# Optimization experiments

Hardware: AMD Instinct MI355X
Metric: run time of the kernel (lower is better)

## Reference

```python
import jax, jax.numpy as jnp
import numpy as np

B, L, C, D, H = 32, 4096, 64, 512, 720
EPS = 1e-5

def _xavier(key, shape):
    fan_in, fan_out = shape
    lim = float(np.sqrt(6.0 / (fan_in + fan_out)))
    return jax.random.uniform(key, shape, minval=-lim, maxval=lim, dtype=jnp.float32)

def setup_inputs() -> dict:
    key = jax.random.key(0)
    ks = jax.random.split(key, 8)
    return {
        "x": jax.random.normal(ks[0], (B, L, C), dtype=jnp.float32),
        "alpha": jnp.full((C,), 0.5, dtype=jnp.float32),
        "rev_w": jnp.ones((C,), dtype=jnp.float32),
        "rev_b": jnp.zeros((C,), dtype=jnp.float32),
        "se_w": _xavier(ks[1], (C, D)), "se_b": jnp.zeros((D,), jnp.float32),
        "sp_w": _xavier(ks[2], (D, C)), "sp_b": jnp.zeros((C,), jnp.float32),
        "st_w": _xavier(ks[3], (L, H)), "st_b": jnp.zeros((H,), jnp.float32),
        "te_w": _xavier(ks[4], (C, D)), "te_b": jnp.zeros((D,), jnp.float32),
        "tp_w": _xavier(ks[5], (D, C)), "tp_b": jnp.zeros((C,), jnp.float32),
        "tt_w": _xavier(ks[6], (L, H)), "tt_b": jnp.zeros((H,), jnp.float32),
    }

def _path(z, ew, eb, pw, pb, tw, tb):
    # z: (B,L,C) -> embed C->D -> (identity backbone) -> proj D->C -> temporal L->H
    h = z @ ew + eb            # (B,L,D)
    h = h @ pw + pb            # (B,L,C)
    h = jnp.einsum('blc,lh->bhc', h, tw) + tb[None, :, None]  # (B,H,C)
    return h

def reference(x, alpha, rev_w, rev_b, se_w, se_b, sp_w, sp_b, st_w, st_b,
              te_w, te_b, tp_w, tp_b, tt_w, tt_b):
    # RevIN norm (stats detached, var unbiased=False)
    mean = jax.lax.stop_gradient(jnp.mean(x, axis=1, keepdims=True))          # (B,1,C)
    stdev = jax.lax.stop_gradient(jnp.sqrt(jnp.var(x, axis=1, keepdims=True) + EPS))
    xn = (x - mean) / stdev * rev_w + rev_b
    # EMA decomposition: trend[t] = a*trend[t-1] + (1-a)*x[t], trend[0]=x[0]
    a = jax.nn.sigmoid(alpha)  # (C,)
    def step(carry, xt):
        nxt = a * carry + (1.0 - a) * xt
        return nxt, nxt
    t0 = xn[:, 0]                                    # (B,C)
    _, tr = jax.lax.scan(step, t0, jnp.swapaxes(xn, 0, 1)[1:])  # (L-1,B,C)
    trend = jnp.swapaxes(jnp.concatenate([t0[None], tr], axis=0), 0, 1)  # (B,L,C)
    seasonal = xn - trend
    out = _path(seasonal, se_w, se_b, sp_w, sp_b, st_w, st_b) \
        + _path(trend,    te_w, te_b, tp_w, tp_b, tt_w, tt_b)   # (B,H,C)
    # RevIN denorm
    out = (out - rev_b) / (rev_w + EPS)
    out = out * stdev + mean
    return out
```

## Files before the change

### kernel.cpp

```cpp
#include <hip/hip_runtime.h>
#include <hip/hip_bf16.h>
#include <string.h>
#include <stdint.h>

typedef __hip_bfloat16 bf16_t;
typedef float f32x4 __attribute__((ext_vector_type(4)));
typedef short bf16x8 __attribute__((ext_vector_type(8)));

#define AS_GLOBAL __attribute__((address_space(1)))
#define AS_LDS    __attribute__((address_space(3)))

static constexpr int Bn = 32, Ln = 4096, Cn = 64, Hn = 720, HPn = 768;
static constexpr float EPSf = 1e-5f;

static constexpr size_t OSR_SLICE = (size_t)Bn * Hn * Cn;

__device__ __forceinline__ short f2bf(float f) {
  bf16_t h = __float2bfloat16(f);
  unsigned short u; memcpy(&u, &h, 2);
  return (short)u;
}

__device__ __forceinline__ float sigm(float v) { return 1.f / (1.f + expf(-v)); }

__global__ void __launch_bounds__(256) k_prep(const float* __restrict__ se_w, const float* __restrict__ sp_w,
                                              const float* __restrict__ se_b, const float* __restrict__ sp_b,
                                              const float* __restrict__ te_w, const float* __restrict__ tp_w,
                                              const float* __restrict__ te_b, const float* __restrict__ tp_b,
                                              float* __restrict__ M, float* __restrict__ cvec) {
  int p = blockIdx.y, dc = blockIdx.x, t = threadIdx.x;
  const float* ew = p ? te_w : se_w;
  const float* pw = p ? tp_w : sp_w;
  const float* eb = p ? te_b : se_b;
  const float* pb = p ? tp_b : sp_b;
  int d0 = dc * 64;
  __shared__ float ews[64][68];
  __shared__ float pws[64][68];
  __shared__ float ebs[64];
#pragma unroll
  for (int q = 0; q < 4; ++q) {
    int fi = t * 4 + q;
    int r = fi >> 4, dd = (fi * 4) & 63;
    *reinterpret_cast<f32x4*>(&ews[r][dd]) = *reinterpret_cast<const f32x4*>(&ew[r * 512 + d0 + dd]);
    int pdd = fi >> 4, c = (fi * 4) & 63;
    *reinterpret_cast<f32x4*>(&pws[pdd][c]) = *reinterpret_cast<const f32x4*>(&pw[(d0 + pdd) * 64 + c]);
  }
  if (t < 64) ebs[t] = eb[d0 + t];
  __syncthreads();
  int r0 = (t >> 4) * 4, c0 = (t & 15) * 4;
  float acc[4][4];
#pragma unroll
  for (int i = 0; i < 4; ++i)
#pragma unroll
    for (int j = 0; j < 4; ++j) acc[i][j] = 0.f;
#pragma unroll 4
  for (int g = 0; g < 16; ++g) {
    int dd = g * 4;
    f32x4 av[4], bv[4];
#pragma unroll
    for (int i = 0; i < 4; ++i) av[i] = *reinterpret_cast<const f32x4*>(&ews[r0 + i][dd]);
#pragma unroll
    for (int d = 0; d < 4; ++d) bv[d] = *reinterpret_cast<const f32x4*>(&pws[dd + d][c0]);
#pragma unroll
    for (int d = 0; d < 4; ++d)
#pragma unroll
      for (int i = 0; i < 4; ++i)
#pragma unroll
        for (int j = 0; j < 4; ++j) acc[i][j] = fmaf(av[i][d], bv[d][j], acc[i][j]);
  }
#pragma unroll
  for (int i = 0; i < 4; ++i)
#pragma unroll
    for (int j = 0; j < 4; ++j)
      atomicAdd(&M[p * 4096 + (r0 + i) * 64 + c0 + j], acc[i][j]);
  if (t < 64) {
    float s = (dc == 0) ? pb[t] : 0.f;
#pragma unroll 8
    for (int dd = 0; dd < 64; ++dd) s = fmaf(ebs[dd], pws[dd][t], s);
    atomicAdd(&cvec[p * 64 + t], s);
  }
}

__global__ void k_wprep(const float* __restrict__ st_w, const float* __restrict__ tt_w,
                        bf16_t* __restrict__ Wt, float* __restrict__ S) {
  int p = blockIdx.z;
  const float* W = p ? tt_w : st_w;
  int l0 = blockIdx.x * 64, h0 = blockIdx.y * 64;
  __shared__ float tile[64][65];
  int row = threadIdx.x >> 6, col = threadIdx.x & 63;
  int h = h0 + col;
  float partial = 0.f;
  for (int r = row; r < 64; r += 4) {
    float v = (h < Hn) ? W[(size_t)(l0 + r) * Hn + h] : 0.f;
    tile[r][col] = v;
    partial += v;
  }
  if (h < Hn) atomicAdd(&S[p * 768 + h], partial);
  __syncthreads();
  for (int a = row; a < 64; a += 4) {
    float v = tile[col][a];
    Wt[(size_t)(p * HPn + h0 + a) * Ln + l0 + col] = __float2bfloat16(v);
  }
}

__global__ void __launch_bounds__(256) k_scanA(const float* __restrict__ x, const float* __restrict__ alpha,
                                               float* __restrict__ Psub, float* __restrict__ Pseg,
                                               float* __restrict__ Ssum, float* __restrict__ Ssq) {
  int b = blockIdx.x, q = threadIdx.y, s = blockIdx.y * 4 + q, t = threadIdx.x;
  int c4 = (t & 15) * 4, sub = t >> 4;
  float a[4], k1[4];
#pragma unroll
  for (int i = 0; i < 4; ++i) { a[i] = sigm(alpha[c4 + i]); k1[i] = 1.f - a[i]; }
  const float* xb = x + ((size_t)b * Ln + s * 64 + sub * 16) * Cn + c4;
  float pr[4] = {0.f, 0.f, 0.f, 0.f}, sm[4] = {0.f, 0.f, 0.f, 0.f}, sq[4] = {0.f, 0.f, 0.f, 0.f};
#pragma unroll
  for (int j = 0; j < 16; ++j) {
    f32x4 v = *reinterpret_cast<const f32x4*>(xb + (size_t)j * Cn);
#pragma unroll
    for (int i = 0; i < 4; ++i) {
      sm[i] += v[i];
      sq[i] = fmaf(v[i], v[i], sq[i]);
      pr[i] = fmaf(a[i], pr[i], k1[i] * v[i]);
    }
  }
  *reinterpret_cast<f32x4*>(&Psub[(((size_t)b * 64 + s) * 4 + sub) * 64 + c4]) =
      (f32x4){pr[0], pr[1], pr[2], pr[3]};
  __shared__ float lp[4][4][64], ls[4][4][64], lq[4][4][64];
#pragma unroll
  for (int i = 0; i < 4; ++i) { lp[q][sub][c4 + i] = pr[i]; ls[q][sub][c4 + i] = sm[i]; lq[q][sub][c4 + i] = sq[i]; }
  __syncthreads();
  int c = t;
  float av = sigm(alpha[c]);
  float a16 = av * av; a16 *= a16; a16 *= a16; a16 *= a16;
  float P = ((lp[q][0][c] * a16 + lp[q][1][c]) * a16 + lp[q][2][c]) * a16 + lp[q][3][c];
  int idx = (b * 64 + s) * 64 + c;
  Pseg[idx] = P;
  Ssum[idx] = ls[q][0][c] + ls[q][1][c] + ls[q][2][c] + ls[q][3][c];
  Ssq[idx]  = lq[q][0][c] + lq[q][1][c] + lq[q][2][c] + lq[q][3][c];
}

__global__ void __launch_bounds__(64) k_scanB(const float* __restrict__ x, const float* __restrict__ alpha,
                                              const float* __restrict__ rev_w, const float* __restrict__ rev_b,
                                              const float* __restrict__ Pseg, const float* __restrict__ Ssum,
                                              const float* __restrict__ Ssq,
                                              float* __restrict__ mean, float* __restrict__ rstd,
                                              float* __restrict__ stdv, float* __restrict__ CarryIn) {
  int b = blockIdx.x, c = threadIdx.x;
  float sm = 0.f, sq = 0.f;
#pragma unroll 8
  for (int s = 0; s < 64; ++s) {
    int idx = (b * 64 + s) * 64 + c;
    sm += Ssum[idx]; sq += Ssq[idx];
  }
  float mn = sm * (1.f / 4096.f);
  float var = sq * (1.f / 4096.f) - mn * mn;
  float sd = sqrtf(var + EPSf);
  float rs = 1.f / sd;
  mean[b * 64 + c] = mn; stdv[b * 64 + c] = sd; rstd[b * 64 + c] = rs;

  float w = rev_w[c], rb = rev_b[c];
  float g = rs * w, d = rb - mn * g;
  float a = sigm(alpha[c]);
  float a2 = a * a, a4 = a2 * a2, a8 = a4 * a4, a16 = a8 * a8, a32 = a16 * a16;
  float a64 = a32 * a32;
  float dk1s = d * (1.f - a64);
  float carry = fmaf(g, x[((size_t)b * Ln) * Cn + c], d);
  for (int so = 0; so < 8; ++so) {
    float pv[8];
#pragma unroll
    for (int i = 0; i < 8; ++i)
      pv[i] = Pseg[((size_t)(b * 64 + so * 8 + i)) * 64 + c];
#pragma unroll
    for (int i = 0; i < 8; ++i) {
      CarryIn[((size_t)(b * 64 + so * 8 + i)) * 64 + c] = carry;
      carry = fmaf(a64, carry, fmaf(g, pv[i], dk1s));
    }
  }
}

__global__ void __launch_bounds__(256) k_scanC(const float* __restrict__ x, const float* __restrict__ alpha,
                                               const float* __restrict__ rev_w, const float* __restrict__ rev_b,
                                               const float* __restrict__ mean, const float* __restrict__ rstd,
                                               const float* __restrict__ CarryIn, const float* __restrict__ Psub,
                                               bf16_t* __restrict__ Zt) {
  int b = blockIdx.x, s = blockIdx.y * 4 + threadIdx.y, t = threadIdx.x;
  int c4 = (t & 15) * 4, sub = t >> 4;
  float g[4], d[4], a[4], k1[4], a16[4], dk[4], tr[4];
#pragma unroll
  for (int i = 0; i < 4; ++i) {
    int c = c4 + i;
    float rs = rstd[b * 64 + c];
    g[i] = rs * rev_w[c]; d[i] = rev_b[c] - mean[b * 64 + c] * g[i];
    a[i] = sigm(alpha[c]); k1[i] = 1.f - a[i];
    float v = a[i] * a[i]; v *= v; v *= v; v *= v;
    a16[i] = v;
    dk[i] = d[i] * (1.f - v);
  }
  f32x4 cs = *reinterpret_cast<const f32x4*>(&CarryIn[((size_t)b * 64 + s) * 64 + c4]);
#pragma unroll
  for (int i = 0; i < 4; ++i) tr[i] = cs[i];
  for (int k = 0; k < sub; ++k) {
    f32x4 p = *reinterpret_cast<const f32x4*>(&Psub[(((size_t)b * 64 + s) * 4 + k) * 64 + c4]);
#pragma unroll
    for (int i = 0; i < 4; ++i) tr[i] = fmaf(a16[i], tr[i], fmaf(g[i], p[i], dk[i]));
  }
  const float* xb = x + ((size_t)b * Ln + s * 64 + sub * 16) * Cn + c4;
  bf16x8 vs[4][2], vt[4][2];
#pragma unroll
  for (int j = 0; j < 16; ++j) {
    f32x4 v = *reinterpret_cast<const f32x4*>(xb + (size_t)j * Cn);
#pragma unroll
    for (int i = 0; i < 4; ++i) {
      float xn = fmaf(g[i], v[i], d[i]);
      tr[i] = fmaf(a[i], tr[i], k1[i] * xn);
      vs[i][j >> 3][j & 7] = f2bf(xn - tr[i]);
      vt[i][j >> 3][j & 7] = f2bf(tr[i]);
    }
  }
#pragma unroll
  for (int i = 0; i < 4; ++i) {
    int c = c4 + i;
    bf16_t* zs = Zt + ((size_t)b * 64 + c) * Ln + s * 64 + sub * 16;
    bf16_t* zt = zs + (size_t)Bn * Cn * Ln;
    *reinterpret_cast<bf16x8*>(zs) = vs[i][0];
    *reinterpret_cast<bf16x8*>(zs + 8) = vs[i][1];
    *reinterpret_cast<bf16x8*>(zt) = vt[i][0];
    *reinterpret_cast<bf16x8*>(zt + 8) = vt[i][1];
  }
}

__device__ __forceinline__ void gload16(const bf16_t* g, bf16_t* l) {
  __builtin_amdgcn_global_load_lds((const AS_GLOBAL uint32_t*)g, (AS_LDS uint32_t*)l, 16, 0, 0);
}

template <int KS>
__global__ void __launch_bounds__(256, 3) k_gemm(const bf16_t* __restrict__ Wt, const bf16_t* __restrict__ Zt,
                                                 float* __restrict__ Osr) {
  int z = blockIdx.z;
  int p = z / KS, kq = z % KS;
  const bf16_t* A  = Wt + (size_t)p * HPn * Ln;
  const bf16_t* Bz = Zt + (size_t)p * (Bn * Cn) * Ln;
  int h0 = blockIdx.y * 128, n0 = blockIdx.x * 128;
  int kbase = kq * (Ln / KS);
  const int NT = (Ln / KS) / 32;
  __shared__ __align__(16) bf16_t Al[3][128 * 32];
  __shared__ __align__(16) bf16_t Bl[3][128 * 32];
  int tid = threadIdx.x, wid = tid >> 6, lane = tid & 63;
  int wr = wid >> 1, wc = wid & 1;
  int fr = lane & 15, hi = lane >> 4;
  int kc = (tid & 3) ^ ((tid >> 3) & 3);
  const bf16_t* abase = A + (size_t)(h0 + (tid >> 2)) * Ln + kbase + kc * 8;
  const bf16_t* bbase = Bz + (size_t)(n0 + (tid >> 2)) * Ln + kbase + kc * 8;

  f32x4 acc[4][4];
#pragma unroll
  for (int i = 0; i < 4; ++i)
#pragma unroll
    for (int j = 0; j < 4; ++j) acc[i][j] = (f32x4){0.f, 0.f, 0.f, 0.f};

  auto STAGE = [&](int bufi, int kt) {
    gload16(abase + (size_t)kt * 32, &Al[bufi][tid * 8]);
    gload16(abase + (size_t)64 * Ln + kt * 32, &Al[bufi][2048 + tid * 8]);
    gload16(bbase + (size_t)kt * 32, &Bl[bufi][tid * 8]);
    gload16(bbase + (size_t)64 * Ln + kt * 32, &Bl[bufi][2048 + tid * 8]);
  };

  int sw8 = (hi ^ ((fr >> 1) & 3)) * 8;
  auto COMPUTE = [&](int bufi) {
    bf16x8 afr[4], bfr[4];
#pragma unroll
    for (int i = 0; i < 4; ++i)
      afr[i] = *reinterpret_cast<const bf16x8*>(&Al[bufi][(wr * 64 + i * 16 + fr) * 32 + sw8]);
#pragma unroll
    for (int j = 0; j < 4; ++j)
      bfr[j] = *reinterpret_cast<const bf16x8*>(&Bl[bufi][(wc * 64 + j * 16 + fr) * 32 + sw8]);
    __builtin_amdgcn_s_setprio(1);
#pragma unroll
    for (int i = 0; i < 4; ++i)
#pragma unroll
      for (int j = 0; j < 4; ++j)
        acc[i][j] = __builtin_amdgcn_mfma_f32_16x16x32_bf16(afr[i], bfr[j], acc[i][j], 0, 0, 0);
    __builtin_amdgcn_s_setprio(0);
  };

  STAGE(0, 0);
  STAGE(1, 1);
  int cur = 0, nx = 2;
  for (int t = 0; t < NT; ++t) {
    __builtin_amdgcn_sched_barrier(0);
    if (t + 1 < NT) { asm volatile("s_waitcnt vmcnt(4)" ::: "memory"); }
    else            { asm volatile("s_waitcnt vmcnt(0)" ::: "memory"); }
    __builtin_amdgcn_s_barrier();
    __builtin_amdgcn_sched_barrier(0);
    if (t + 2 < NT) STAGE(nx, t + 2);
    COMPUTE(cur);
    cur = (cur == 2) ? 0 : cur + 1;
    nx  = (nx == 2) ? 0 : nx + 1;
  }

#pragma unroll
  for (int i = 0; i < 4; ++i) {
#pragma unroll
    for (int j = 0; j < 4; ++j) {
#pragma unroll
      for (int r = 0; r < 4; ++r) {
        int m = wr * 64 + i * 16 + hi * 4 + r;
        int h = h0 + m;
        if (h < Hn) {
          int n = n0 + wc * 64 + j * 16 + fr;
          int bidx = n >> 6, c = n & 63;
          Osr[(((size_t)z * Bn + bidx) * Hn + h) * Cn + c] = acc[i][j][r];
        }
      }
    }
  }
}

template <int KS>
__global__ void __launch_bounds__(256) k_epi(const float* __restrict__ Osr, const float* __restrict__ M,
                                             const float* __restrict__ cvec, const float* __restrict__ S,
                                             const float* __restrict__ st_b, const float* __restrict__ tt_b,
                                             const float* __restrict__ rev_w, const float* __restrict__ rev_b,
                                             const float* __restrict__ mean, const float* __restrict__ stdv,
                                             float* __restrict__ out) {
  __shared__ float Msh[2][64][64];
  __shared__ float rowS[4][64];
  __shared__ float rowT[4][64];
  int t = threadIdx.x;
  for (int i = t; i < 8192; i += 256) ((float*)Msh)[i] = M[i];
  int g = t >> 6, c = t & 63;
  float w = rev_w[c], rb = rev_b[c];
  float cs = cvec[c], ct = cvec[64 + c];
  int base = blockIdx.x * 16;
  for (int it = 0; it < 4; ++it) {
    int r = base + it * 4 + g;
    int b = r / 720, h = r % 720;
    __syncthreads();
    float vs = 0.f, vt = 0.f;
#pragma unroll
    for (int kq = 0; kq < KS; ++kq) {
      vs += Osr[(((size_t)kq * Bn + b) * Hn + h) * Cn + c];
      vt += Osr[(((size_t)(KS + kq) * Bn + b) * Hn + h) * Cn + c];
    }
    rowS[g][c] = vs;
    rowT[g][c] = vt;
    __syncthreads();
    float acc = cs * S[h] + ct * S[768 + h] + st_b[h] + tt_b[h];
    for (int cp = 0; cp < 64; ++cp)
      acc = fmaf(rowS[g][cp], Msh[0][cp][c], fmaf(rowT[g][cp], Msh[1][cp][c], acc));
    float o = (acc - rb) / (w + EPSf) * stdv[b * Cn + c] + mean[b * Cn + c];
    out[(size_t)r * 64 + c] = o;
  }
}

extern "C" void kernel_launch(void* const* d_in, const int* in_sizes, int n_in,
                              void* d_out, int out_size, void* d_ws, size_t ws_size,
                              hipStream_t stream) {
  const float* x     = (const float*)d_in[0];
  const float* alpha = (const float*)d_in[1];
  const float* rev_w = (const float*)d_in[2];
  const float* rev_b = (const float*)d_in[3];
  const float* se_w  = (const float*)d_in[4];
  const float* se_b  = (const float*)d_in[5];
  const float* sp_w  = (const float*)d_in[6];
  const float* sp_b  = (const float*)d_in[7];
  const float* st_w  = (const float*)d_in[8];
  const float* st_b  = (const float*)d_in[9];
  const float* te_w  = (const float*)d_in[10];
  const float* te_b  = (const float*)d_in[11];
  const float* tp_w  = (const float*)d_in[12];
  const float* tp_b  = (const float*)d_in[13];
  const float* tt_w  = (const float*)d_in[14];
  const float* tt_b  = (const float*)d_in[15];
  float* out = (float*)d_out;

  const size_t SZ_WT  = (size_t)2 * HPn * Ln * 2;
  const size_t SZ_ZT  = (size_t)2 * Bn * Cn * Ln * 2;
  const size_t SZ_SEG = (size_t)Bn * 64 * 64 * 4;
  const size_t SZ_M   = 2 * 64 * 64 * 4;
  const size_t SZ_CV  = 2 * 64 * 4;
  const size_t SZ_S   = 2 * 768 * 4;
  const size_t TAIL   = SZ_M + SZ_CV + SZ_S + 3 * (size_t)Bn * Cn * 4;

  const size_t NEED4 = SZ_WT + SZ_ZT + 8 * OSR_SLICE * 4 + TAIL;
  const int KS = (ws_size >= NEED4) ? 4 : 1;
  const size_t SZ_OSR = (size_t)(2 * KS) * OSR_SLICE * 4;

  char* ws = (char*)d_ws;
  bf16_t* Wt   = (bf16_t*)(ws);
  bf16_t* Zt   = (bf16_t*)(ws + SZ_WT);
  float*  Osr  = (float*)(ws + SZ_WT + SZ_ZT);
  float*  Psub  = Osr;
  float*  Pseg  = (float*)((char*)Psub + 4 * SZ_SEG);
  float*  Ssum  = (float*)((char*)Pseg + SZ_SEG);
  float*  Ssq   = (float*)((char*)Ssum + SZ_SEG);
  float*  Carry = (float*)((char*)Ssq + SZ_SEG);
  char* tail = ws + SZ_WT + SZ_ZT + SZ_OSR;
  float* Mbuf = (float*)tail;                 tail += SZ_M;
  float* cvec = (float*)tail;                 tail += SZ_CV;
  float* S    = (float*)tail;                 tail += SZ_S;
  float* mean = (float*)tail;                 tail += (size_t)Bn * Cn * 4;
  float* rstd = (float*)tail;                 tail += (size_t)Bn * Cn * 4;
  float* stdv = (float*)tail;

  hipMemsetAsync(Mbuf, 0, SZ_M + SZ_CV + SZ_S, stream);

  k_prep<<<dim3(8, 2), 256, 0, stream>>>(se_w, sp_w, se_b, sp_b, te_w, tp_w, te_b, tp_b, Mbuf, cvec);
  k_wprep<<<dim3(64, 12, 2), 256, 0, stream>>>(st_w, tt_w, Wt, S);
  k_scanA<<<dim3(32, 16), dim3(64, 4), 0, stream>>>(x, alpha, Psub, Pseg, Ssum, Ssq);
  k_scanB<<<32, 64, 0, stream>>>(x, alpha, rev_w, rev_b, Pseg, Ssum, Ssq, mean, rstd, stdv, Carry);
  k_scanC<<<dim3(32, 16), dim3(64, 4), 0, stream>>>(x, alpha, rev_w, rev_b, mean, rstd, Carry, Psub, Zt);
  if (KS == 4) {
    k_gemm<4><<<dim3(16, 6, 8), 256, 0, stream>>>(Wt, Zt, Osr);
    k_epi<4><<<1440, 256, 0, stream>>>(Osr, Mbuf, cvec, S, st_b, tt_b, rev_w, rev_b, mean, stdv, out);
  } else {
    k_gemm<1><<<dim3(16, 6, 2), 256, 0, stream>>>(Wt, Zt, Osr);
    k_epi<1><<<1440, 256, 0, stream>>>(Osr, Mbuf, cvec, S, st_b, tt_b, rev_w, rev_b, mean, stdv, out);
  }
}
```

Before: 117.9 us.

## Pre-swizzle weight operand into MFMA fragment layout and load directly to registers

The weight-prep kernel now writes the transposed bf16 weights in a fragment-major tiled layout matching the 16x16x32 MFMA A-operand, so each lane's 8 elements are contiguous. The GEMM drops the LDS staging buffer for A and loads A fragments straight from global memory into registers, double-buffered across iterations, with waitcnt values adjusted. This cuts LDS traffic and LDS footprint for A but duplicates A global loads across the two column-waves and relies on the hand-tuned vmcnt counts staying correct.

New measurement: 115.6 us. Within noise of the previous version (-1.9%).

```diff
diff --git a/kernel.cpp b/kernel.cpp
--- a/kernel.cpp
+++ b/kernel.cpp
@@ -97,9 +97,19 @@
   }
   if (h < Hn) atomicAdd(&S[p * 768 + h], partial);
   __syncthreads();
-  for (int a = row; a < 64; a += 4) {
-    float v = tile[col][a];
-    Wt[(size_t)(p * HPn + h0 + a) * Ln + l0 + col] = __float2bfloat16(v);
+  short* AF = (short*)Wt + (size_t)p * HPn * Ln;
+#pragma unroll
+  for (int u = 0; u < 2; ++u) {
+    int uid = u * 256 + threadIdx.x;
+    int ln = uid & 63, ktl = (uid >> 6) & 1, htl = uid >> 7;
+    int fr = ln & 15, hi = ln >> 4;
+    int ll = ktl * 32 + hi * 8;
+    int hh = htl * 16 + fr;
+    bf16x8 v;
+#pragma unroll
+    for (int e = 0; e < 8; ++e) v[e] = f2bf(tile[ll + e][hh]);
+    size_t ht = (size_t)(h0 >> 4) + htl, ktg = (size_t)(l0 >> 5) + ktl;
+    *reinterpret_cast<bf16x8*>(&AF[((ht * 128 + ktg) << 9) + ((size_t)ln << 3)]) = v;
   }
 }
 
@@ -238,19 +248,18 @@
                                                  float* __restrict__ Osr) {
   int z = blockIdx.z;
   int p = z / KS, kq = z % KS;
-  const bf16_t* A  = Wt + (size_t)p * HPn * Ln;
+  const short* AF = (const short*)Wt + (size_t)p * HPn * Ln;
   const bf16_t* Bz = Zt + (size_t)p * (Bn * Cn) * Ln;
   int h0 = blockIdx.y * 128, n0 = blockIdx.x * 128;
   int kbase = kq * (Ln / KS);
   const int NT = (Ln / KS) / 32;
-  __shared__ __align__(16) bf16_t Al[3][128 * 32];
   __shared__ __align__(16) bf16_t Bl[3][128 * 32];
   int tid = threadIdx.x, wid = tid >> 6, lane = tid & 63;
   int wr = wid >> 1, wc = wid & 1;
   int fr = lane & 15, hi = lane >> 4;
   int kc = (tid & 3) ^ ((tid >> 3) & 3);
-  const bf16_t* abase = A + (size_t)(h0 + (tid >> 2)) * Ln + kbase + kc * 8;
   const bf16_t* bbase = Bz + (size_t)(n0 + (tid >> 2)) * Ln + kbase + kc * 8;
+  const short* abase = AF + ((((size_t)(h0 >> 4) + wr * 4) * 128 + (kbase >> 5)) << 9) + ((size_t)lane << 3);
 
   f32x4 acc[4][4];
 #pragma unroll
@@ -258,19 +267,19 @@
 #pragma unroll
     for (int j = 0; j < 4; ++j) acc[i][j] = (f32x4){0.f, 0.f, 0.f, 0.f};
 
-  auto STAGE = [&](int bufi, int kt) {
-    gload16(abase + (size_t)kt * 32, &Al[bufi][tid * 8]);
-    gload16(abase + (size_t)64 * Ln + kt * 32, &Al[bufi][2048 + tid * 8]);
+  auto STAGE_B = [&](int bufi, int kt) {
     gload16(bbase + (size_t)kt * 32, &Bl[bufi][tid * 8]);
     gload16(bbase + (size_t)64 * Ln + kt * 32, &Bl[bufi][2048 + tid * 8]);
   };
+  auto ALOAD = [&](bf16x8 (&dst)[4], int kt) {
+#pragma unroll
+    for (int i = 0; i < 4; ++i)
+      dst[i] = *reinterpret_cast<const bf16x8*>(abase + (((size_t)i * 128 + kt) << 9));
+  };
 
   int sw8 = (hi ^ ((fr >> 1) & 3)) * 8;
-  auto COMPUTE = [&](int bufi) {
-    bf16x8 afr[4], bfr[4];
-#pragma unroll
-    for (int i = 0; i < 4; ++i)
-      afr[i] = *reinterpret_cast<const bf16x8*>(&Al[bufi][(wr * 64 + i * 16 + fr) * 32 + sw8]);
+  auto COMPUTE = [&](int bufi, const bf16x8 (&af)[4]) {
+    bf16x8 bfr[4];
 #pragma unroll
     for (int j = 0; j < 4; ++j)
       bfr[j] = *reinterpret_cast<const bf16x8*>(&Bl[bufi][(wc * 64 + j * 16 + fr) * 32 + sw8]);
@@ -279,23 +288,34 @@
     for (int i = 0; i < 4; ++i)
 #pragma unroll
       for (int j = 0; j < 4; ++j)
-        acc[i][j] = __builtin_amdgcn_mfma_f32_16x16x32_bf16(afr[i], bfr[j], acc[i][j], 0, 0, 0);
+        acc[i][j] = __builtin_amdgcn_mfma_f32_16x16x32_bf16(af[i], bfr[j], acc[i][j], 0, 0, 0);
     __builtin_amdgcn_s_setprio(0);
   };
 
-  STAGE(0, 0);
-  STAGE(1, 1);
-  int cur = 0, nx = 2;
-  for (int t = 0; t < NT; ++t) {
+  bf16x8 aA[4], aB[4];
+  STAGE_B(0, 0);
+  STAGE_B(1, 1);
+  ALOAD(aA, 0);
+
+  auto ITER = [&](int t, int cur, int nx, const bf16x8 (&acur)[4], bf16x8 (&anxt)[4]) {
     __builtin_amdgcn_sched_barrier(0);
-    if (t + 1 < NT) { asm volatile("s_waitcnt vmcnt(4)" ::: "memory"); }
-    else            { asm volatile("s_waitcnt vmcnt(0)" ::: "memory"); }
+    if (t + 1 < NT) { asm volatile("s_waitcnt vmcnt(6)" ::: "memory"); }
+    else            { asm volatile("s_waitcnt vmcnt(4)" ::: "memory"); }
     __builtin_amdgcn_s_barrier();
     __builtin_amdgcn_sched_barrier(0);
-    if (t + 2 < NT) STAGE(nx, t + 2);
-    COMPUTE(cur);
-    cur = (cur == 2) ? 0 : cur + 1;
-    nx  = (nx == 2) ? 0 : nx + 1;
+    if (t + 2 < NT) STAGE_B(nx, t + 2);
+    if (t + 1 < NT) ALOAD(anxt, t + 1);
+    COMPUTE(cur, acur);
+  };
+
+  int cur = 0;
+  for (int t = 0; t < NT; t += 2) {
+    int c1 = (cur == 2) ? 0 : cur + 1;
+    int nx0 = (c1 == 2) ? 0 : c1 + 1;
+    int nx1 = cur;
+    ITER(t,     cur, nx0, aA, aB);
+    ITER(t + 1, c1,  nx1, aB, aA);
+    cur = nx0;
   }
 
 #pragma unroll
```
